# Performance work log

Hardware: AMD Instinct MI355X
Metric: run time of the kernel (lower is better)

Reference implementation:

```python
import jax, jax.numpy as jnp
import numpy as np

N = 100000   # nodes
E = 1600000  # edges (before self loops)
B = 64       # graphs in batch
F_IN = 128
H1, C1 = 8, 8   # conv1: heads=8, per-head channels=8 -> concat out 64
H2, C2 = 1, 8   # conv2: heads=1, out=8, concat=False


def gat_conv(x, src, dst, W, att_src, att_dst, bias, H, C, concat, n_nodes):
    """PyG GATConv (shared src/dst weight, leaky_relu slope 0.2, segment softmax).
    src/dst already include self loops. x: [N, F], W: [F, H*C],
    att_src/att_dst: [1, H, C], bias: [H*C] or [C]."""
    xh = (x @ W).reshape(n_nodes, H, C)                      # [N, H, C]
    a_src = jnp.sum(xh * att_src, axis=-1)                   # [N, H]
    a_dst = jnp.sum(xh * att_dst, axis=-1)                   # [N, H]
    alpha = jax.nn.leaky_relu(a_src[src] + a_dst[dst], 0.2)  # [E', H]
    # numerically stable segment softmax over incoming edges of each dst node
    amax = jax.ops.segment_max(jax.lax.stop_gradient(alpha), dst, num_segments=n_nodes)
    ex = jnp.exp(alpha - amax[dst])
    denom = jax.ops.segment_sum(ex, dst, num_segments=n_nodes)
    alpha = ex / (denom[dst] + 1e-16)                        # [E', H]
    msg = xh[src] * alpha[..., None]                         # [E', H, C]
    out = jax.ops.segment_sum(msg, dst, num_segments=n_nodes)  # [N, H, C]
    out = out.reshape(n_nodes, H * C) if concat else out.mean(axis=1)
    return out + bias


def setup_inputs() -> dict:
    key = jax.random.key(0)
    ks = jax.random.split(key, 12)
    x = jax.random.normal(ks[0], (N, F_IN), dtype=jnp.float32)
    edge_index = jax.random.randint(ks[1], (2, E), 0, N, dtype=jnp.int32)
    batch = jnp.sort(jax.random.randint(ks[2], (N,), 0, B, dtype=jnp.int32))
    g = 0.1
    W1 = jax.random.normal(ks[3], (F_IN, H1 * C1), dtype=jnp.float32) * g
    a1_src = jax.random.normal(ks[4], (1, H1, C1), dtype=jnp.float32) * g
    a1_dst = jax.random.normal(ks[5], (1, H1, C1), dtype=jnp.float32) * g
    b1 = jnp.zeros((H1 * C1,), dtype=jnp.float32)
    W2 = jax.random.normal(ks[6], (H1 * C1, H2 * C2), dtype=jnp.float32) * g
    a2_src = jax.random.normal(ks[7], (1, H2, C2), dtype=jnp.float32) * g
    a2_dst = jax.random.normal(ks[8], (1, H2, C2), dtype=jnp.float32) * g
    b2 = jnp.zeros((C2,), dtype=jnp.float32)
    return {"x": x, "edge_index": edge_index, "batch": batch,
            "W1": W1, "a1_src": a1_src, "a1_dst": a1_dst, "b1": b1,
            "W2": W2, "a2_src": a2_src, "a2_dst": a2_dst, "b2": b2}


def reference(x, edge_index, batch, W1, a1_src, a1_dst, b1, W2, a2_src, a2_dst, b2):
    # add self loops (PyG GATConv default)
    loop = jnp.arange(N, dtype=edge_index.dtype)
    src = jnp.concatenate([edge_index[0], loop])
    dst = jnp.concatenate([edge_index[1], loop])
    # eval mode: dropouts are identity
    h = gat_conv(x, src, dst, W1, a1_src, a1_dst, b1, H1, C1, True, N)
    h = jax.nn.elu(h)
    h = gat_conv(h, src, dst, W2, a2_src, a2_dst, b2, H2, C2, False, N)
    # global mean pool over graphs
    sums = jax.ops.segment_sum(h, batch, num_segments=B)          # [B, C2]
    cnt = jax.ops.segment_sum(jnp.ones((N,), h.dtype), batch, num_segments=B)
    return sums / jnp.maximum(cnt, 1.0)[:, None]
```

## Files before the change

kernel.cpp:

```cpp
#include <hip/hip_runtime.h>
#include <hip/hip_bf16.h>

#define BIN_SHIFT 8
#define BIN_NODES 256
#define BIN_CAP   8192
#define EPT       16

typedef float v2f __attribute__((ext_vector_type(2)));

__device__ __forceinline__ float leaky02(float a) { return fmaxf(a, 0.2f * a); }
__device__ __forceinline__ unsigned short f2bf(float f) {
    __hip_bfloat16 h = __float2bfloat16(f);
    return *(unsigned short*)&h;
}
__device__ __forceinline__ float bflo(unsigned u) { return __uint_as_float(u << 16); }
__device__ __forceinline__ float bfhi(unsigned u) { return __uint_as_float(u & 0xffff0000u); }
__device__ __forceinline__ v2f bf2(unsigned u) {
    v2f r; r.x = __uint_as_float(u << 16); r.y = __uint_as_float(u & 0xffff0000u); return r;
}

__global__ __launch_bounds__(512) void k1_kernel(const float* __restrict__ x,
                                                 const float* __restrict__ W,
                                                 const float* __restrict__ a1s,
                                                 const float* __restrict__ a1d,
                                                 const int* __restrict__ ei,
                                                 __hip_bfloat16* __restrict__ xh,
                                                 float* __restrict__ asrc,
                                                 float* __restrict__ adst,
                                                 int* __restrict__ cur,
                                                 unsigned* __restrict__ binned,
                                                 int N, int E, int Etot, int NB, int NBB) {
    __shared__ float ws[128 * 64];
    __shared__ float xs[64][132];
    __shared__ int bcnt[512];
    int tid = threadIdx.x;
    if (blockIdx.x < NBB) {
        bcnt[tid] = 0;
        __syncthreads();
        long long base = (long long)blockIdx.x * 512 * EPT;
#pragma unroll 4
        for (int i = 0; i < EPT; ++i) {
            long long e = base + i * 512 + tid;
            if (e < Etot) {
                int dst = (e < E) ? ei[E + e] : (int)(e - E);
                atomicAdd(&bcnt[dst >> BIN_SHIFT], 1);
            }
        }
        __syncthreads();
        for (int b = tid; b < NB; b += 512) {
            int c = bcnt[b];
            bcnt[b] = c ? atomicAdd(&cur[b], c) : 0;
        }
        __syncthreads();
#pragma unroll 4
        for (int i = 0; i < EPT; ++i) {
            long long e = base + i * 512 + tid;
            if (e < Etot) {
                int src, dst;
                if (e < E) { src = ei[e]; dst = ei[E + e]; }
                else       { src = dst = (int)(e - E); }
                int bin = dst >> BIN_SHIFT;
                int p = atomicAdd(&bcnt[bin], 1);
                if (p < BIN_CAP)
                    binned[(size_t)bin * BIN_CAP + p] = ((unsigned)(dst & (BIN_NODES - 1)) << 24) | (unsigned)src;
            }
        }
        return;
    }
    int gb = blockIdx.x - NBB;
    for (int i = tid; i < 2048; i += 512) ((float4*)ws)[i] = ((const float4*)W)[i];
    int row0 = gb * 64;
    for (int i = tid; i < 64 * 32; i += 512) {
        int r = i >> 5, c4 = i & 31;
        int row = row0 + r;
        float4 v = make_float4(0.f, 0.f, 0.f, 0.f);
        if (row < N) v = ((const float4*)x)[row * 32 + c4];
        float* p = &xs[r][c4 * 4];
        p[0] = v.x; p[1] = v.y; p[2] = v.z; p[3] = v.w;
    }
    __syncthreads();
    int tc = tid & 15, tr = tid >> 4;
    float acc[2][4] = {};
#pragma unroll 4
    for (int k = 0; k < 128; ++k) {
        float a0 = xs[tr * 2][k];
        float a1 = xs[tr * 2 + 1][k];
        float4 b = *(const float4*)&ws[k * 64 + tc * 4];
        acc[0][0] += a0 * b.x; acc[0][1] += a0 * b.y; acc[0][2] += a0 * b.z; acc[0][3] += a0 * b.w;
        acc[1][0] += a1 * b.x; acc[1][1] += a1 * b.y; acc[1][2] += a1 * b.z; acc[1][3] += a1 * b.w;
    }
    float4 sv = ((const float4*)a1s)[tc];
    float4 dv = ((const float4*)a1d)[tc];
    int head = tc >> 1;
#pragma unroll
    for (int r = 0; r < 2; ++r) {
        int row = row0 + tr * 2 + r;
        if (row < N) {
            uint2 o;
            o.x = (unsigned)f2bf(acc[r][0]) | ((unsigned)f2bf(acc[r][1]) << 16);
            o.y = (unsigned)f2bf(acc[r][2]) | ((unsigned)f2bf(acc[r][3]) << 16);
            *(uint2*)(xh + (size_t)row * 64 + tc * 4) = o;
        }
        float sp = acc[r][0] * sv.x + acc[r][1] * sv.y + acc[r][2] * sv.z + acc[r][3] * sv.w;
        float dp = acc[r][0] * dv.x + acc[r][1] * dv.y + acc[r][2] * dv.z + acc[r][3] * dv.w;
        sp += __shfl_xor(sp, 1);
        dp += __shfl_xor(dp, 1);
        if (!(tc & 1) && row < N) {
            asrc[row * 8 + head] = sp;
            adst[row * 8 + head] = dp;
        }
    }
}

__global__ __launch_bounds__(256) void binC_kernel(const int* __restrict__ cur,
                                                   const unsigned* __restrict__ binned,
                                                   int* __restrict__ rowptr,
                                                   int* __restrict__ esrc,
                                                   int N, int Etot, int NB) {
    int bin = blockIdx.x;
    int tid = threadIdx.x;
    __shared__ int psum[256];
    __shared__ int sc[256];
    __shared__ int ndc[256];
    int s = 0;
    for (int i = tid; i < bin; i += 256) s += cur[i];
    psum[tid] = s;
    __syncthreads();
    for (int off = 128; off > 0; off >>= 1) {
        if (tid < off) psum[tid] += psum[tid + off];
        __syncthreads();
    }
    int bbase = psum[0];
    int cnt = cur[bin];
    ndc[tid] = 0;
    __syncthreads();
    const unsigned* bp = binned + (size_t)bin * BIN_CAP;
    for (int i = tid; i < cnt; i += 256)
        atomicAdd(&ndc[bp[i] >> 24], 1);
    __syncthreads();
    int v = ndc[tid];
    sc[tid] = v;
    __syncthreads();
    for (int off = 1; off < 256; off <<= 1) {
        int t = (tid >= off) ? sc[tid - off] : 0;
        __syncthreads();
        sc[tid] += t;
        __syncthreads();
    }
    int excl = sc[tid] - v;
    int node = bin * BIN_NODES + tid;
    if (node < N) rowptr[node] = bbase + excl;
    if (bin == NB - 1 && tid == 0) rowptr[N] = Etot;
    ndc[tid] = excl;
    __syncthreads();
    for (int i = tid; i < cnt; i += 256) {
        unsigned w = bp[i];
        int p = atomicAdd(&ndc[w >> 24], 1);
        esrc[bbase + p] = (int)(w & 0xFFFFFFu);
    }
}

__global__ __launch_bounds__(256) void agg1_kernel(const int* __restrict__ rowptr,
                                                   const int* __restrict__ esrc,
                                                   const float* __restrict__ asrc,
                                                   const float* __restrict__ adst,
                                                   const __hip_bfloat16* __restrict__ xh,
                                                   const float* __restrict__ b1,
                                                   __hip_bfloat16* __restrict__ h1, int N) {
    int node = blockIdx.x * 4 + (threadIdx.x >> 6);
    if (node >= N) return;
    int lane = threadIdx.x & 63;
    unsigned slot = (unsigned)(lane >> 3), h = (unsigned)(lane & 7);
    float adh = adst[(unsigned)node * 8u + h];
    unsigned start = (unsigned)rowptr[node];
    int len = rowptr[node + 1] - (int)start;
    const uint4* xh4 = (const uint4*)xh;
    float d = 0.f;
    v2f acc0 = {0.f, 0.f}, acc1 = {0.f, 0.f}, acc2 = {0.f, 0.f}, acc3 = {0.f, 0.f};
    for (int kb = 0; kb < len; kb += 32) {
        int k0 = kb + (int)slot;
        bool ok0 = k0 < len, ok1 = k0 + 8 < len, ok2 = k0 + 16 < len, ok3 = k0 + 24 < len;
        unsigned s0 = ok0 ? (unsigned)esrc[start + k0] : 0u;
        unsigned s1 = ok1 ? (unsigned)esrc[start + k0 + 8] : 0u;
        unsigned s2 = ok2 ? (unsigned)esrc[start + k0 + 16] : 0u;
        unsigned s3 = ok3 ? (unsigned)esrc[start + k0 + 24] : 0u;
        float a0 = ok0 ? asrc[s0 * 8u + h] : -1e30f;
        float a1 = ok1 ? asrc[s1 * 8u + h] : -1e30f;
        float a2 = ok2 ? asrc[s2 * 8u + h] : -1e30f;
        float a3 = ok3 ? asrc[s3 * 8u + h] : -1e30f;
        uint4 u0 = xh4[s0 * 8u + h];
        uint4 u1 = xh4[s1 * 8u + h];
        uint4 u2 = xh4[s2 * 8u + h];
        uint4 u3 = xh4[s3 * 8u + h];
        float p0 = __expf(leaky02(a0 + adh));
        float p1 = __expf(leaky02(a1 + adh));
        float p2 = __expf(leaky02(a2 + adh));
        float p3 = __expf(leaky02(a3 + adh));
        d += (p0 + p1) + (p2 + p3);
        acc0 += bf2(u0.x) * p0; acc1 += bf2(u0.y) * p0;
        acc2 += bf2(u0.z) * p0; acc3 += bf2(u0.w) * p0;
        acc0 += bf2(u1.x) * p1; acc1 += bf2(u1.y) * p1;
        acc2 += bf2(u1.z) * p1; acc3 += bf2(u1.w) * p1;
        acc0 += bf2(u2.x) * p2; acc1 += bf2(u2.y) * p2;
        acc2 += bf2(u2.z) * p2; acc3 += bf2(u2.w) * p2;
        acc0 += bf2(u3.x) * p3; acc1 += bf2(u3.y) * p3;
        acc2 += bf2(u3.z) * p3; acc3 += bf2(u3.w) * p3;
    }
#pragma unroll
    for (int off = 8; off < 64; off <<= 1) {
        d += __shfl_xor(d, off);
        acc0.x += __shfl_xor(acc0.x, off); acc0.y += __shfl_xor(acc0.y, off);
        acc1.x += __shfl_xor(acc1.x, off); acc1.y += __shfl_xor(acc1.y, off);
        acc2.x += __shfl_xor(acc2.x, off); acc2.y += __shfl_xor(acc2.y, off);
        acc3.x += __shfl_xor(acc3.x, off); acc3.y += __shfl_xor(acc3.y, off);
    }
    float vals[8] = {acc0.x, acc0.y, acc1.x, acc1.y, acc2.x, acc2.y, acc3.x, acc3.y};
    float hv = vals[0];
#pragma unroll
    for (int c = 1; c < 8; ++c) hv = ((int)slot == c) ? vals[c] : hv;
    int f = (int)(h * 8u + slot);
    hv = hv / (d + 1e-16f) + b1[f];
    hv = hv > 0.f ? hv : __expf(hv) - 1.0f;
    float hvp = __shfl(hv, ((lane & 7) << 3) | (lane >> 3));
    h1[(unsigned)node * 64u + (unsigned)lane] = __float2bfloat16(hvp);
}

__global__ __launch_bounds__(256) void gemm2h_kernel(const __hip_bfloat16* __restrict__ h1,
                                                     const float* __restrict__ W2,
                                                     const float* __restrict__ a2s,
                                                     const float* __restrict__ a2d,
                                                     __hip_bfloat16* __restrict__ xh2,
                                                     float* __restrict__ asrc2,
                                                     float* __restrict__ adst2, int N) {
    __shared__ float w2s[512];
    __shared__ float aa[16];
    int tid = threadIdx.x;
    for (int i = tid; i < 512; i += 256) w2s[i] = W2[i];
    if (tid < 8) aa[tid] = a2s[tid];
    else if (tid < 16) aa[tid] = a2d[tid - 8];
    __syncthreads();
    unsigned n = blockIdx.x * 256u + (unsigned)tid;
    if (n >= (unsigned)N) return;
    const uint4* hp = (const uint4*)h1 + n * 8u;
    float q[8] = {};
#pragma unroll
    for (int j = 0; j < 8; ++j) {
        uint4 u = hp[j];
        float hv[8] = {bflo(u.x), bfhi(u.x), bflo(u.y), bfhi(u.y),
                       bflo(u.z), bfhi(u.z), bflo(u.w), bfhi(u.w)};
#pragma unroll
        for (int e = 0; e < 8; ++e) {
            int f = j * 8 + e;
            float4 wa = *(const float4*)&w2s[f * 8];
            float4 wb = *(const float4*)&w2s[f * 8 + 4];
            q[0] += hv[e] * wa.x; q[1] += hv[e] * wa.y;
            q[2] += hv[e] * wa.z; q[3] += hv[e] * wa.w;
            q[4] += hv[e] * wb.x; q[5] += hv[e] * wb.y;
            q[6] += hv[e] * wb.z; q[7] += hv[e] * wb.w;
        }
    }
    uint4 o;
    o.x = (unsigned)f2bf(q[0]) | ((unsigned)f2bf(q[1]) << 16);
    o.y = (unsigned)f2bf(q[2]) | ((unsigned)f2bf(q[3]) << 16);
    o.z = (unsigned)f2bf(q[4]) | ((unsigned)f2bf(q[5]) << 16);
    o.w = (unsigned)f2bf(q[6]) | ((unsigned)f2bf(q[7]) << 16);
    *((uint4*)xh2 + n) = o;
    float s2 = 0.f, d2 = 0.f;
#pragma unroll
    for (int c = 0; c < 8; ++c) { s2 += q[c] * aa[c]; d2 += q[c] * aa[8 + c]; }
    asrc2[n] = s2;
    adst2[n] = d2;
}

__global__ __launch_bounds__(256) void agg2_pool_kernel(const int* __restrict__ rowptr,
                                                        const int* __restrict__ esrc,
                                                        const float* __restrict__ asrc2,
                                                        const float* __restrict__ adst2,
                                                        const __hip_bfloat16* __restrict__ xh2,
                                                        const float* __restrict__ b2,
                                                        const int* __restrict__ batch,
                                                        float* __restrict__ pool,
                                                        float* __restrict__ cnt, int N, int B) {
    __shared__ float ps[64 * 8];
    __shared__ float cs[64];
    int tid = threadIdx.x;
    for (int i = tid; i < 512; i += 256) ps[i] = 0.f;
    if (tid < 64) cs[tid] = 0.f;
    __syncthreads();
    int node = blockIdx.x * 32 + (tid >> 3);
    int slot = tid & 7;
    if (node < N) {
        float adh = adst2[node];
        unsigned start = (unsigned)rowptr[node];
        int len = rowptr[node + 1] - (int)start;
        const uint4* x4 = (const uint4*)xh2;
        float d = 0.f;
        v2f acc0 = {0.f, 0.f}, acc1 = {0.f, 0.f}, acc2 = {0.f, 0.f}, acc3 = {0.f, 0.f};
        for (int kb = 0; kb < len; kb += 32) {
            int k0 = kb + slot;
            bool ok0 = k0 < len, ok1 = k0 + 8 < len, ok2 = k0 + 16 < len, ok3 = k0 + 24 < len;
            unsigned s0 = ok0 ? (unsigned)esrc[start + k0] : 0u;
            unsigned s1 = ok1 ? (unsigned)esrc[start + k0 + 8] : 0u;
            unsigned s2 = ok2 ? (unsigned)esrc[start + k0 + 16] : 0u;
            unsigned s3 = ok3 ? (unsigned)esrc[start + k0 + 24] : 0u;
            float a0 = ok0 ? asrc2[s0] : -1e30f;
            float a1 = ok1 ? asrc2[s1] : -1e30f;
            float a2 = ok2 ? asrc2[s2] : -1e30f;
            float a3 = ok3 ? asrc2[s3] : -1e30f;
            uint4 u0 = x4[s0];
            uint4 u1 = x4[s1];
            uint4 u2 = x4[s2];
            uint4 u3 = x4[s3];
            float p0 = __expf(leaky02(a0 + adh));
            float p1 = __expf(leaky02(a1 + adh));
            float p2 = __expf(leaky02(a2 + adh));
            float p3 = __expf(leaky02(a3 + adh));
            d += (p0 + p1) + (p2 + p3);
            acc0 += bf2(u0.x) * p0; acc1 += bf2(u0.y) * p0;
            acc2 += bf2(u0.z) * p0; acc3 += bf2(u0.w) * p0;
            acc0 += bf2(u1.x) * p1; acc1 += bf2(u1.y) * p1;
            acc2 += bf2(u1.z) * p1; acc3 += bf2(u1.w) * p1;
            acc0 += bf2(u2.x) * p2; acc1 += bf2(u2.y) * p2;
            acc2 += bf2(u2.z) * p2; acc3 += bf2(u2.w) * p2;
            acc0 += bf2(u3.x) * p3; acc1 += bf2(u3.y) * p3;
            acc2 += bf2(u3.z) * p3; acc3 += bf2(u3.w) * p3;
        }
#pragma unroll
        for (int off = 1; off < 8; off <<= 1) {
            d += __shfl_xor(d, off);
            acc0.x += __shfl_xor(acc0.x, off); acc0.y += __shfl_xor(acc0.y, off);
            acc1.x += __shfl_xor(acc1.x, off); acc1.y += __shfl_xor(acc1.y, off);
            acc2.x += __shfl_xor(acc2.x, off); acc2.y += __shfl_xor(acc2.y, off);
            acc3.x += __shfl_xor(acc3.x, off); acc3.y += __shfl_xor(acc3.y, off);
        }
        float vals[8] = {acc0.x, acc0.y, acc1.x, acc1.y, acc2.x, acc2.y, acc3.x, acc3.y};
        float v = vals[0];
#pragma unroll
        for (int c = 1; c < 8; ++c) v = (slot == c) ? vals[c] : v;
        v = v / (d + 1e-16f) + b2[slot];
        int b = batch[node];
        atomicAdd(&ps[b * 8 + slot], v);
        if (slot == 0) atomicAdd(&cs[b], 1.0f);
    }
    __syncthreads();
    for (int i = tid; i < 512; i += 256)
        if (ps[i] != 0.f) atomicAdd(&pool[i], ps[i]);
    if (tid < 64 && cs[tid] != 0.f) atomicAdd(&cnt[tid], cs[tid]);
}

__global__ __launch_bounds__(256) void final_kernel(const float* __restrict__ pool,
                                                    const float* __restrict__ cnt,
                                                    float* __restrict__ out, int B) {
    int idx = blockIdx.x * 256 + threadIdx.x;
    if (idx >= B * 8) return;
    out[idx] = pool[idx] / fmaxf(cnt[idx >> 3], 1.0f);
}

extern "C" void kernel_launch(void* const* d_in, const int* in_sizes, int n_in,
                              void* d_out, int out_size, void* d_ws, size_t ws_size,
                              hipStream_t stream) {
    const float* x   = (const float*)d_in[0];
    const int*   ei  = (const int*)d_in[1];
    const int*   bat = (const int*)d_in[2];
    const float* W1  = (const float*)d_in[3];
    const float* a1s = (const float*)d_in[4];
    const float* a1d = (const float*)d_in[5];
    const float* b1  = (const float*)d_in[6];
    const float* W2  = (const float*)d_in[7];
    const float* a2s = (const float*)d_in[8];
    const float* a2d = (const float*)d_in[9];
    const float* b2  = (const float*)d_in[10];
    float* out = (float*)d_out;

    const int N = in_sizes[0] / 128;
    const int E = in_sizes[1] / 2;
    const int B = out_size / 8;
    const int Etot = E + N;
    const int NB = (N + BIN_NODES - 1) / BIN_NODES;
    const int NBB = (Etot + 512 * EPT - 1) / (512 * EPT);
    const int NG = (N + 63) / 64;

    float* wsp = (float*)d_ws;
    __hip_bfloat16* xh1 = (__hip_bfloat16*)wsp;
    float* asrc1  = wsp + (size_t)N * 32;
    float* adst1  = asrc1 + (size_t)N * 8;
    __hip_bfloat16* h1 = (__hip_bfloat16*)(adst1 + (size_t)N * 8);
    __hip_bfloat16* xh2 = (__hip_bfloat16*)(adst1 + (size_t)N * 40);
    float* asrc2  = adst1 + (size_t)N * 44;
    float* adst2  = asrc2 + (size_t)N;
    int*   rowptr = (int*)(adst2 + (size_t)N);
    int*   esrc   = rowptr + (size_t)N + 8;
    unsigned* binned = (unsigned*)(esrc + (size_t)Etot);
    int*   cur    = (int*)(binned + (size_t)NB * BIN_CAP);
    float* pool   = (float*)(cur + NB);
    float* cnt    = pool + (size_t)B * 8;
    size_t zbytes = ((size_t)NB + 9 * (size_t)B) * 4;
    hipMemsetAsync(cur, 0, zbytes, stream);

    k1_kernel<<<dim3(NBB + NG), dim3(512), 0, stream>>>(x, W1, a1s, a1d, ei,
                                                        xh1, asrc1, adst1,
                                                        cur, binned, N, E, Etot, NB, NBB);
    binC_kernel<<<dim3(NB), dim3(256), 0, stream>>>(cur, binned, rowptr, esrc, N, Etot, NB);
    agg1_kernel<<<dim3((N + 3) / 4), dim3(256), 0, stream>>>(rowptr, esrc, asrc1, adst1, xh1, b1, h1, N);
    gemm2h_kernel<<<dim3((N + 255) / 256), dim3(256), 0, stream>>>(h1, W2, a2s, a2d, xh2, asrc2, adst2, N);
    agg2_pool_kernel<<<dim3((N + 31) / 32), dim3(256), 0, stream>>>(rowptr, esrc, asrc2, adst2,
                                                                    xh2, b2, bat, pool, cnt, N, B);
    final_kernel<<<dim3((B * 8 + 255) / 256), dim3(256), 0, stream>>>(pool, cnt, out, B);
}
```

Measured before the change: 161.0 us.

## Recompute source attention logits from gathered features instead of storing them

Stops precomputing and storing per-node source attention scores in both GEMM kernels. The aggregation kernels now compute each score on the fly as a dot product of the gathered bf16 feature row with att_src, which removes one dependent random gather per edge. The first GEMM also drops its shared-memory staging of x and reads x rows straight from global memory. The trade-off is more ALU work per edge, and the scores now come from bf16-rounded features, which can shift numerics slightly.

```diff
diff --git a/kernel.cpp b/kernel.cpp
--- a/kernel.cpp
+++ b/kernel.cpp
@@ -21,17 +21,14 @@
 
 __global__ __launch_bounds__(512) void k1_kernel(const float* __restrict__ x,
                                                  const float* __restrict__ W,
-                                                 const float* __restrict__ a1s,
                                                  const float* __restrict__ a1d,
                                                  const int* __restrict__ ei,
                                                  __hip_bfloat16* __restrict__ xh,
-                                                 float* __restrict__ asrc,
                                                  float* __restrict__ adst,
                                                  int* __restrict__ cur,
                                                  unsigned* __restrict__ binned,
                                                  int N, int E, int Etot, int NB, int NBB) {
     __shared__ float ws[128 * 64];
-    __shared__ float xs[64][132];
     __shared__ int bcnt[512];
     int tid = threadIdx.x;
     if (blockIdx.x < NBB) {
@@ -69,46 +66,45 @@
     }
     int gb = blockIdx.x - NBB;
     for (int i = tid; i < 2048; i += 512) ((float4*)ws)[i] = ((const float4*)W)[i];
-    int row0 = gb * 64;
-    for (int i = tid; i < 64 * 32; i += 512) {
-        int r = i >> 5, c4 = i & 31;
-        int row = row0 + r;
-        float4 v = make_float4(0.f, 0.f, 0.f, 0.f);
-        if (row < N) v = ((const float4*)x)[row * 32 + c4];
-        float* p = &xs[r][c4 * 4];
-        p[0] = v.x; p[1] = v.y; p[2] = v.z; p[3] = v.w;
-    }
     __syncthreads();
     int tc = tid & 15, tr = tid >> 4;
+    int row0 = gb * 64 + tr * 2;
+    int row1 = row0 + 1;
+    int rr0 = min(row0, N - 1), rr1 = min(row1, N - 1);
+    bool ok0 = row0 < N, ok1 = row1 < N;
+    const float4* xp0 = (const float4*)x + (size_t)rr0 * 32;
+    const float4* xp1 = (const float4*)x + (size_t)rr1 * 32;
     float acc[2][4] = {};
-#pragma unroll 4
-    for (int k = 0; k < 128; ++k) {
-        float a0 = xs[tr * 2][k];
-        float a1 = xs[tr * 2 + 1][k];
-        float4 b = *(const float4*)&ws[k * 64 + tc * 4];
-        acc[0][0] += a0 * b.x; acc[0][1] += a0 * b.y; acc[0][2] += a0 * b.z; acc[0][3] += a0 * b.w;
-        acc[1][0] += a1 * b.x; acc[1][1] += a1 * b.y; acc[1][2] += a1 * b.z; acc[1][3] += a1 * b.w;
-    }
-    float4 sv = ((const float4*)a1s)[tc];
+#pragma unroll 2
+    for (int kt = 0; kt < 32; ++kt) {
+        float4 a0 = xp0[kt];
+        float4 a1 = xp1[kt];
+        float a0j[4] = {a0.x, a0.y, a0.z, a0.w};
+        float a1j[4] = {a1.x, a1.y, a1.z, a1.w};
+#pragma unroll
+        for (int j = 0; j < 4; ++j) {
+            float4 b = *(const float4*)&ws[(kt * 4 + j) * 64 + tc * 4];
+            acc[0][0] += a0j[j] * b.x; acc[0][1] += a0j[j] * b.y;
+            acc[0][2] += a0j[j] * b.z; acc[0][3] += a0j[j] * b.w;
+            acc[1][0] += a1j[j] * b.x; acc[1][1] += a1j[j] * b.y;
+            acc[1][2] += a1j[j] * b.z; acc[1][3] += a1j[j] * b.w;
+        }
+    }
     float4 dv = ((const float4*)a1d)[tc];
     int head = tc >> 1;
+    bool okr[2] = {ok0, ok1};
 #pragma unroll
     for (int r = 0; r < 2; ++r) {
-        int row = row0 + tr * 2 + r;
-        if (row < N) {
+        int row = row0 + r;
+        if (okr[r]) {
             uint2 o;
             o.x = (unsigned)f2bf(acc[r][0]) | ((unsigned)f2bf(acc[r][1]) << 16);
             o.y = (unsigned)f2bf(acc[r][2]) | ((unsigned)f2bf(acc[r][3]) << 16);
             *(uint2*)(xh + (size_t)row * 64 + tc * 4) = o;
         }
-        float sp = acc[r][0] * sv.x + acc[r][1] * sv.y + acc[r][2] * sv.z + acc[r][3] * sv.w;
         float dp = acc[r][0] * dv.x + acc[r][1] * dv.y + acc[r][2] * dv.z + acc[r][3] * dv.w;
-        sp += __shfl_xor(sp, 1);
         dp += __shfl_xor(dp, 1);
-        if (!(tc & 1) && row < N) {
-            asrc[row * 8 + head] = sp;
-            adst[row * 8 + head] = dp;
-        }
+        if (!(tc & 1) && okr[r]) adst[row * 8 + head] = dp;
     }
 }
 
@@ -162,7 +158,7 @@
 
 __global__ __launch_bounds__(256) void agg1_kernel(const int* __restrict__ rowptr,
                                                    const int* __restrict__ esrc,
-                                                   const float* __restrict__ asrc,
+                                                   const float* __restrict__ a1s,
                                                    const float* __restrict__ adst,
                                                    const __hip_bfloat16* __restrict__ xh,
                                                    const float* __restrict__ b1,
@@ -172,6 +168,9 @@
     int lane = threadIdx.x & 63;
     unsigned slot = (unsigned)(lane >> 3), h = (unsigned)(lane & 7);
     float adh = adst[(unsigned)node * 8u + h];
+    const float* wsh = a1s + h * 8u;
+    v2f w01 = {wsh[0], wsh[1]}, w23 = {wsh[2], wsh[3]};
+    v2f w45 = {wsh[4], wsh[5]}, w67 = {wsh[6], wsh[7]};
     unsigned start = (unsigned)rowptr[node];
     int len = rowptr[node + 1] - (int)start;
     const uint4* xh4 = (const uint4*)xh;
@@ -184,27 +183,27 @@
         unsigned s1 = ok1 ? (unsigned)esrc[start + k0 + 8] : 0u;
         unsigned s2 = ok2 ? (unsigned)esrc[start + k0 + 16] : 0u;
         unsigned s3 = ok3 ? (unsigned)esrc[start + k0 + 24] : 0u;
-        float a0 = ok0 ? asrc[s0 * 8u + h] : -1e30f;
-        float a1 = ok1 ? asrc[s1 * 8u + h] : -1e30f;
-        float a2 = ok2 ? asrc[s2 * 8u + h] : -1e30f;
-        float a3 = ok3 ? asrc[s3 * 8u + h] : -1e30f;
         uint4 u0 = xh4[s0 * 8u + h];
         uint4 u1 = xh4[s1 * 8u + h];
         uint4 u2 = xh4[s2 * 8u + h];
         uint4 u3 = xh4[s3 * 8u + h];
-        float p0 = __expf(leaky02(a0 + adh));
-        float p1 = __expf(leaky02(a1 + adh));
-        float p2 = __expf(leaky02(a2 + adh));
-        float p3 = __expf(leaky02(a3 + adh));
+        v2f v00 = bf2(u0.x), v01 = bf2(u0.y), v02 = bf2(u0.z), v03 = bf2(u0.w);
+        v2f v10 = bf2(u1.x), v11 = bf2(u1.y), v12 = bf2(u1.z), v13 = bf2(u1.w);
+        v2f v20 = bf2(u2.x), v21 = bf2(u2.y), v22 = bf2(u2.z), v23 = bf2(u2.w);
+        v2f v30 = bf2(u3.x), v31 = bf2(u3.y), v32 = bf2(u3.z), v33 = bf2(u3.w);
+        v2f av0 = v00 * w01 + v01 * w23 + v02 * w45 + v03 * w67;
+        v2f av1 = v10 * w01 + v11 * w23 + v12 * w45 + v13 * w67;
+        v2f av2 = v20 * w01 + v21 * w23 + v22 * w45 + v23 * w67;
+        v2f av3 = v30 * w01 + v31 * w23 + v32 * w45 + v33 * w67;
+        float p0 = ok0 ? __expf(leaky02(av0.x + av0.y + adh)) : 0.f;
+        float p1 = ok1 ? __expf(leaky02(av1.x + av1.y + adh)) : 0.f;
+        float p2 = ok2 ? __expf(leaky02(av2.x + av2.y + adh)) : 0.f;
+        float p3 = ok3 ? __expf(leaky02(av3.x + av3.y + adh)) : 0.f;
         d += (p0 + p1) + (p2 + p3);
-        acc0 += bf2(u0.x) * p0; acc1 += bf2(u0.y) * p0;
-        acc2 += bf2(u0.z) * p0; acc3 += bf2(u0.w) * p0;
-        acc0 += bf2(u1.x) * p1; acc1 += bf2(u1.y) * p1;
-        acc2 += bf2(u1.z) * p1; acc3 += bf2(u1.w) * p1;
-        acc0 += bf2(u2.x) * p2; acc1 += bf2(u2.y) * p2;
-        acc2 += bf2(u2.z) * p2; acc3 += bf2(u2.w) * p2;
-        acc0 += bf2(u3.x) * p3; acc1 += bf2(u3.y) * p3;
-        acc2 += bf2(u3.z) * p3; acc3 += bf2(u3.w) * p3;
+        acc0 += v00 * p0; acc1 += v01 * p0; acc2 += v02 * p0; acc3 += v03 * p0;
+        acc0 += v10 * p1; acc1 += v11 * p1; acc2 += v12 * p1; acc3 += v13 * p1;
+        acc0 += v20 * p2; acc1 += v21 * p2; acc2 += v22 * p2; acc3 += v23 * p2;
+        acc0 += v30 * p3; acc1 += v31 * p3; acc2 += v32 * p3; acc3 += v33 * p3;
     }
 #pragma unroll
     for (int off = 8; off < 64; off <<= 1) {
@@ -227,17 +226,14 @@
 
 __global__ __launch_bounds__(256) void gemm2h_kernel(const __hip_bfloat16* __restrict__ h1,
                                                      const float* __restrict__ W2,
-                                                     const float* __restrict__ a2s,
                                                      const float* __restrict__ a2d,
                                                      __hip_bfloat16* __restrict__ xh2,
-                                                     float* __restrict__ asrc2,
                                                      float* __restrict__ adst2, int N) {
     __shared__ float w2s[512];
-    __shared__ float aa[16];
+    __shared__ float aa[8];
     int tid = threadIdx.x;
     for (int i = tid; i < 512; i += 256) w2s[i] = W2[i];
-    if (tid < 8) aa[tid] = a2s[tid];
-    else if (tid < 16) aa[tid] = a2d[tid - 8];
+    if (tid < 8) aa[tid] = a2d[tid];
     __syncthreads();
     unsigned n = blockIdx.x * 256u + (unsigned)tid;
     if (n >= (unsigned)N) return;
@@ -265,16 +261,15 @@
     o.z = (unsigned)f2bf(q[4]) | ((unsigned)f2bf(q[5]) << 16);
     o.w = (unsigned)f2bf(q[6]) | ((unsigned)f2bf(q[7]) << 16);
     *((uint4*)xh2 + n) = o;
-    float s2 = 0.f, d2 = 0.f;
-#pragma unroll
-    for (int c = 0; c < 8; ++c) { s2 += q[c] * aa[c]; d2 += q[c] * aa[8 + c]; }
-    asrc2[n] = s2;
+    float d2 = 0.f;
+#pragma unroll
+    for (int c = 0; c < 8; ++c) d2 += q[c] * aa[c];
     adst2[n] = d2;
 }
 
 __global__ __launch_bounds__(256) void agg2_pool_kernel(const int* __restrict__ rowptr,
                                                         const int* __restrict__ esrc,
-                                                        const float* __restrict__ asrc2,
+                                                        const float* __restrict__ a2s,
                                                         const float* __restrict__ adst2,
                                                         const __hip_bfloat16* __restrict__ xh2,
                                                         const float* __restrict__ b2,
@@ -291,6 +286,8 @@
     int slot = tid & 7;
     if (node < N) {
         float adh = adst2[node];
+        v2f w01 = {a2s[0], a2s[1]}, w23 = {a2s[2], a2s[3]};
+        v2f w45 = {a2s[4], a2s[5]}, w67 = {a2s[6], a2s[7]};
         unsigned start = (unsigned)rowptr[node];
         int len = rowptr[node + 1] - (int)start;
         const uint4* x4 = (const uint4*)xh2;
@@ -303,27 +300,27 @@
             unsigned s1 = ok1 ? (unsigned)esrc[start + k0 + 8] : 0u;
             unsigned s2 = ok2 ? (unsigned)esrc[start + k0 + 16] : 0u;
             unsigned s3 = ok3 ? (unsigned)esrc[start + k0 + 24] : 0u;
-            float a0 = ok0 ? asrc2[s0] : -1e30f;
-            float a1 = ok1 ? asrc2[s1] : -1e30f;
-            float a2 = ok2 ? asrc2[s2] : -1e30f;
-            float a3 = ok3 ? asrc2[s3] : -1e30f;
             uint4 u0 = x4[s0];
             uint4 u1 = x4[s1];
             uint4 u2 = x4[s2];
             uint4 u3 = x4[s3];
-            float p0 = __expf(leaky02(a0 + adh));
-            float p1 = __expf(leaky02(a1 + adh));
-            float p2 = __expf(leaky02(a2 + adh));
-            float p3 = __expf(leaky02(a3 + adh));
+            v2f v00 = bf2(u0.x), v01 = bf2(u0.y), v02 = bf2(u0.z), v03 = bf2(u0.w);
+            v2f v10 = bf2(u1.x), v11 = bf2(u1.y), v12 = bf2(u1.z), v13 = bf2(u1.w);
+            v2f v20 = bf2(u2.x), v21 = bf2(u2.y), v22 = bf2(u2.z), v23 = bf2(u2.w);
+            v2f v30 = bf2(u3.x), v31 = bf2(u3.y), v32 = bf2(u3.z), v33 = bf2(u3.w);
+            v2f av0 = v00 * w01 + v01 * w23 + v02 * w45 + v03 * w67;
+            v2f av1 = v10 * w01 + v11 * w23 + v12 * w45 + v13 * w67;
+            v2f av2 = v20 * w01 + v21 * w23 + v22 * w45 + v23 * w67;
+            v2f av3 = v30 * w01 + v31 * w23 + v32 * w45 + v33 * w67;
+            float p0 = ok0 ? __expf(leaky02(av0.x + av0.y + adh)) : 0.f;
+            float p1 = ok1 ? __expf(leaky02(av1.x + av1.y + adh)) : 0.f;
+            float p2 = ok2 ? __expf(leaky02(av2.x + av2.y + adh)) : 0.f;
+            float p3 = ok3 ? __expf(leaky02(av3.x + av3.y + adh)) : 0.f;
             d += (p0 + p1) + (p2 + p3);
-            acc0 += bf2(u0.x) * p0; acc1 += bf2(u0.y) * p0;
-            acc2 += bf2(u0.z) * p0; acc3 += bf2(u0.w) * p0;
-            acc0 += bf2(u1.x) * p1; acc1 += bf2(u1.y) * p1;
-            acc2 += bf2(u1.z) * p1; acc3 += bf2(u1.w) * p1;
-            acc0 += bf2(u2.x) * p2; acc1 += bf2(u2.y) * p2;
-            acc2 += bf2(u2.z) * p2; acc3 += bf2(u2.w) * p2;
-            acc0 += bf2(u3.x) * p3; acc1 += bf2(u3.y) * p3;
-            acc2 += bf2(u3.z) * p3; acc3 += bf2(u3.w) * p3;
+            acc0 += v00 * p0; acc1 += v01 * p0; acc2 += v02 * p0; acc3 += v03 * p0;
+            acc0 += v10 * p1; acc1 += v11 * p1; acc2 += v12 * p1; acc3 += v13 * p1;
+            acc0 += v20 * p2; acc1 += v21 * p2; acc2 += v22 * p2; acc3 += v23 * p2;
+            acc0 += v30 * p3; acc1 += v31 * p3; acc2 += v32 * p3; acc3 += v33 * p3;
         }
 #pragma unroll
         for (int off = 1; off < 8; off <<= 1) {
@@ -382,12 +379,10 @@
 
     float* wsp = (float*)d_ws;
     __hip_bfloat16* xh1 = (__hip_bfloat16*)wsp;
-    float* asrc1  = wsp + (size_t)N * 32;
-    float* adst1  = asrc1 + (size_t)N * 8;
+    float* adst1  = wsp + (size_t)N * 32;
     __hip_bfloat16* h1 = (__hip_bfloat16*)(adst1 + (size_t)N * 8);
     __hip_bfloat16* xh2 = (__hip_bfloat16*)(adst1 + (size_t)N * 40);
-    float* asrc2  = adst1 + (size_t)N * 44;
-    float* adst2  = asrc2 + (size_t)N;
+    float* adst2  = adst1 + (size_t)N * 44;
     int*   rowptr = (int*)(adst2 + (size_t)N);
     int*   esrc   = rowptr + (size_t)N + 8;
     unsigned* binned = (unsigned*)(esrc + (size_t)Etot);
@@ -397,13 +392,13 @@
     size_t zbytes = ((size_t)NB + 9 * (size_t)B) * 4;
     hipMemsetAsync(cur, 0, zbytes, stream);
 
-    k1_kernel<<<dim3(NBB + NG), dim3(512), 0, stream>>>(x, W1, a1s, a1d, ei,
-                                                        xh1, asrc1, adst1,
+    k1_kernel<<<dim3(NBB + NG), dim3(512), 0, stream>>>(x, W1, a1d, ei,
+                                                        xh1, adst1,
                                                         cur, binned, N, E, Etot, NB, NBB);
     binC_kernel<<<dim3(NB), dim3(256), 0, stream>>>(cur, binned, rowptr, esrc, N, Etot, NB);
-    agg1_kernel<<<dim3((N + 3) / 4), dim3(256), 0, stream>>>(rowptr, esrc, asrc1, adst1, xh1, b1, h1, N);
-    gemm2h_kernel<<<dim3((N + 255) / 256), dim3(256), 0, stream>>>(h1, W2, a2s, a2d, xh2, asrc2, adst2, N);
-    agg2_pool_kernel<<<dim3((N + 31) / 32), dim3(256), 0, stream>>>(rowptr, esrc, asrc2, adst2,
+    agg1_kernel<<<dim3((N + 3) / 4), dim3(256), 0, stream>>>(rowptr, esrc, a1s, adst1, xh1, b1, h1, N);
+    gemm2h_kernel<<<dim3((N + 255) / 256), dim3(256), 0, stream>>>(h1, W2, a2d, xh2, adst2, N);
+    agg2_pool_kernel<<<dim3((N + 31) / 32), dim3(256), 0, stream>>>(rowptr, esrc, a2s, adst2,
                                                                     xh2, b2, bat, pool, cnt, N, B);
     final_kernel<<<dim3((B * 8 + 255) / 256), dim3(256), 0, stream>>>(pool, cnt, out, B);
 }
```

Measured after the change: 153.4 us. -4.7%, faster.
